# Kernel optimization log

Hardware: AMD Instinct MI355X
Metric: run time of the kernel (lower is better)

Reference implementation:

```python
import jax, jax.numpy as jnp
import numpy as np

N_NODES = 100000
N_EDGES = 1600000
EMB = 64       # embedding_dim
HID = 128      # hidden_channels
N_GRAPHS = 512
N_TASKS = 128
ATOM_VOCAB = 119
BOND_VOCAB = 16


def setup_inputs() -> dict:
    key = jax.random.key(0)
    ks = jax.random.split(key, 24)
    s = 0.02
    inp = {
        'x_idx': jax.random.randint(ks[0], (N_NODES,), 0, ATOM_VOCAB),
        'edge_index': jax.random.randint(ks[1], (2, N_EDGES), 0, N_NODES),
        'edge_attr_idx': jax.random.randint(ks[2], (N_EDGES,), 0, BOND_VOCAB),
        'batch': jnp.sort(jax.random.randint(ks[3], (N_NODES,), 0, N_GRAPHS)),
        'atom_emb': jax.random.normal(ks[4], (ATOM_VOCAB, EMB), jnp.float32) * s,
        'bond_emb': jax.random.normal(ks[5], (BOND_VOCAB, EMB), jnp.float32) * s,
        'w_edge0': jax.random.normal(ks[6], (EMB, EMB), jnp.float32) * s,
        'b_edge0': jnp.zeros((EMB,), jnp.float32),
        'w1_0': jax.random.normal(ks[7], (EMB, HID), jnp.float32) * s,
        'b1_0': jnp.zeros((HID,), jnp.float32),
        'w2_0': jax.random.normal(ks[8], (HID, HID), jnp.float32) * s,
        'b2_0': jnp.zeros((HID,), jnp.float32),
        'w_edge1': jax.random.normal(ks[9], (EMB, HID), jnp.float32) * s,
        'b_edge1': jnp.zeros((HID,), jnp.float32),
        'w1_1': jax.random.normal(ks[10], (HID, HID), jnp.float32) * s,
        'b1_1': jnp.zeros((HID,), jnp.float32),
        'w2_1': jax.random.normal(ks[11], (HID, HID), jnp.float32) * s,
        'b2_1': jnp.zeros((HID,), jnp.float32),
        'lin1_w': jax.random.normal(ks[12], (HID, HID), jnp.float32) * s,
        'lin1_b': jnp.zeros((HID,), jnp.float32),
        'lin2_w': jax.random.normal(ks[13], (HID, N_TASKS), jnp.float32) * s,
        'lin2_b': jnp.zeros((N_TASKS,), jnp.float32),
    }
    return inp


def _gine_conv(x, e, src, dst, we, be, w1, b1, w2, b2):
    # message: relu(x_j + Linear(edge_attr)); aggregate: scatter-add at dst
    msg = jax.nn.relu(x[src] + e @ we + be)            # [E, in_dim]
    agg = jax.ops.segment_sum(msg, dst, num_segments=N_NODES)
    h = x + agg                                        # (1+eps)*x with eps=0
    h = jax.nn.elu(h @ w1 + b1) @ w2 + b2              # GINE nn MLP
    return jax.nn.elu(h)                               # outer F.elu


def reference(x_idx, edge_index, edge_attr_idx, batch,
              atom_emb, bond_emb,
              w_edge0, b_edge0, w1_0, b1_0, w2_0, b2_0,
              w_edge1, b_edge1, w1_1, b1_1, w2_1, b2_1,
              lin1_w, lin1_b, lin2_w, lin2_b):
    x = atom_emb[x_idx]                                # [N, EMB]
    e = bond_emb[edge_attr_idx]                        # [E, EMB]
    src, dst = edge_index[0], edge_index[1]            # flow: source->target
    x = _gine_conv(x, e, src, dst, w_edge0, b_edge0, w1_0, b1_0, w2_0, b2_0)
    x = _gine_conv(x, e, src, dst, w_edge1, b_edge1, w1_1, b1_1, w2_1, b2_1)
    hg = jax.ops.segment_sum(x, batch, num_segments=N_GRAPHS)  # global_add_pool
    hg = jax.nn.relu(hg @ lin1_w + lin1_b)
    return hg @ lin2_w + lin2_b                        # [G, num_tasks]
```

## Files before the change

kernel.cpp:

```cpp
#include <hip/hip_runtime.h>
#include <hip/hip_bf16.h>

static const int NN = 100000;
static const int NE = 1600000;
static const int NG = 512;
static const int NB = 391;
static const int NBLK = 98;

typedef __attribute__((ext_vector_type(8))) short shortx8;
typedef __attribute__((ext_vector_type(4))) float floatx4;

__device__ __forceinline__ float bf2f(unsigned short u) {
  union { unsigned int i; float f; } v; v.i = ((unsigned int)u) << 16; return v.f;
}
__device__ __forceinline__ unsigned short f2bf(float f) {
  union { float f; unsigned int i; } v; v.f = f;
  return (unsigned short)((v.i + 0x7FFFu + ((v.i >> 16) & 1u)) >> 16);
}

__global__ void k_bhist(const int* __restrict__ dst, int* __restrict__ part) {
  __shared__ int cnt[NB];
  for (int i = threadIdx.x; i < NB; i += 256) cnt[i] = 0;
  __syncthreads();
  int base = blockIdx.x * 16384;
  for (int k = 0; k < 64; ++k) {
    int e = base + k * 256 + threadIdx.x;
    if (e < NE) atomicAdd(&cnt[dst[e] >> 8], 1);
  }
  __syncthreads();
  for (int i = threadIdx.x; i < NB; i += 256) part[i * NBLK + blockIdx.x] = cnt[i];
}

__global__ void k_bscan(const int* __restrict__ part, int* __restrict__ bo,
                        int* __restrict__ bcursor, int* __restrict__ offs,
                        unsigned int* __restrict__ csr0, unsigned int* __restrict__ csr1) {
  __shared__ int sh[512];
  int t = threadIdx.x;
  int c0 = 0, c1 = 0;
  if (t < NB) { const int* p = part + t * NBLK; for (int k = 0; k < NBLK; ++k) c0 += p[k]; }
  int u = t + 256;
  if (u < NB) { const int* p = part + u * NBLK; for (int k = 0; k < NBLK; ++k) c1 += p[k]; }
  sh[t] = c0; sh[t + 256] = c1;
  __syncthreads();
  for (int d = 1; d < 512; d <<= 1) {
    int v0 = (t >= d) ? sh[t - d] : 0;
    int v1 = (t + 256 >= d) ? sh[t + 256 - d] : 0;
    __syncthreads();
    sh[t] += v0; sh[t + 256] += v1;
    __syncthreads();
  }
  if (t < NB) { int e0 = sh[t] - c0; bo[t] = e0; bcursor[t] = e0; }
  if (u < NB) { int e0 = sh[u] - c1; bo[u] = e0; bcursor[u] = e0; }
  if (t == 0) offs[NN] = NE;
  if (t < 8) { csr0[NE + t] = 0u; csr1[NE + t] = 0u; }
}

__global__ void k_bin(const int* __restrict__ src, const int* __restrict__ dstp,
                      const int* __restrict__ ea, const int* __restrict__ x_idx,
                      int* __restrict__ bcursor, uint2* __restrict__ pairs) {
  __shared__ int cnt[512];
  __shared__ int incl[512];
  __shared__ int cur[NB];
  __shared__ int rbase[NB];
  __shared__ uint2 stage[4096];
  int t = threadIdx.x;
  int e0 = blockIdx.x * 4096;
  int ecnt = NE - e0; if (ecnt > 4096) ecnt = 4096;
  cnt[t] = 0; cnt[t + 256] = 0;
  __syncthreads();
  for (int k = 0; k < 16; ++k) {
    int i = k * 256 + t;
    if (i < ecnt) atomicAdd(&cnt[dstp[e0 + i] >> 8], 1);
  }
  __syncthreads();
  incl[t] = cnt[t]; incl[t + 256] = cnt[t + 256];
  __syncthreads();
  for (int d = 1; d < 512; d <<= 1) {
    int v0 = (t >= d) ? incl[t - d] : 0;
    int v1 = (t + 256 >= d) ? incl[t + 256 - d] : 0;
    __syncthreads();
    incl[t] += v0; incl[t + 256] += v1;
    __syncthreads();
  }
  if (t < NB) { cur[t] = incl[t] - cnt[t]; if (cnt[t]) rbase[t] = atomicAdd(&bcursor[t], cnt[t]); }
  int u = t + 256;
  if (u < NB) { cur[u] = incl[u] - cnt[u]; if (cnt[u]) rbase[u] = atomicAdd(&bcursor[u], cnt[u]); }
  __syncthreads();
  for (int k = 0; k < 16; ++k) {
    int i = k * 256 + t;
    if (i < ecnt) {
      int e = e0 + i;
      int d = dstp[e];
      int s = src[e];
      unsigned int pk = (unsigned int)s | ((unsigned int)(x_idx[s] * 16 + ea[e]) << 17);
      int p = atomicAdd(&cur[d >> 8], 1);
      stage[p] = make_uint2((unsigned int)d, pk);
    }
  }
  __syncthreads();
  for (int j = t; j < ecnt; j += 256) {
    int lo = 0, hi = NB - 1;
    while (lo < hi) { int mid = (lo + hi) >> 1; if (incl[mid] > j) hi = mid; else lo = mid + 1; }
    int excl = incl[lo] - cnt[lo];
    pairs[rbase[lo] + (j - excl)] = stage[j];
  }
}

__global__ void k_fine(const uint2* __restrict__ pairs, const int* __restrict__ bo,
                       int* __restrict__ offs,
                       unsigned int* __restrict__ csr0, unsigned int* __restrict__ csr1) {
  __shared__ int cnt[256];
  __shared__ int incl[256];
  __shared__ int cur[256];
  int b = blockIdx.x;
  int t = threadIdx.x;
  int start = bo[b];
  int end = (b == NB - 1) ? NE : bo[b + 1];
  int base_n = b << 8;
  cnt[t] = 0;
  __syncthreads();
  for (int j = start + t; j < end; j += 256)
    atomicAdd(&cnt[(int)pairs[j].x - base_n], 1);
  __syncthreads();
  incl[t] = cnt[t];
  __syncthreads();
  for (int d = 1; d < 256; d <<= 1) {
    int v = (t >= d) ? incl[t - d] : 0;
    __syncthreads();
    incl[t] += v;
    __syncthreads();
  }
  int excl = incl[t] - cnt[t];
  cur[t] = excl;
  int node = base_n + t;
  if (node < NN) offs[node] = start + excl;
  __syncthreads();
  for (int j = start + t; j < end; j += 256) {
    uint2 p = pairs[j];
    int pos = start + atomicAdd(&cur[(int)p.x - base_n], 1);
    unsigned int pk = p.y;
    unsigned int idx17 = pk >> 17;
    csr0[pos] = idx17 << 8;
    csr1[pos] = ((pk & 0x1FFFFu) << 8) | (idx17 & 15u);
  }
}

__global__ void k_prep(const float* __restrict__ bond,
                       const float* __restrict__ we0, const float* __restrict__ be0,
                       const float* __restrict__ we1, const float* __restrict__ be1,
                       const float* __restrict__ atom,
                       float* __restrict__ et1, float* __restrict__ M0,
                       const float* __restrict__ s0, const float* __restrict__ s1,
                       const float* __restrict__ s2, const float* __restrict__ s3,
                       const float* __restrict__ s4, const float* __restrict__ s5,
                       unsigned short* __restrict__ d0, unsigned short* __restrict__ d1,
                       unsigned short* __restrict__ d2, unsigned short* __restrict__ d3,
                       unsigned short* __restrict__ d4, unsigned short* __restrict__ d5) {
  int blk = blockIdx.x, t = threadIdx.x;
  if (blk < 8) {
    int i = blk * 256 + t;
    int b = i >> 7, c = i & 127;
    float acc = be1[c];
    for (int k = 0; k < 64; ++k) acc += bond[b * 64 + k] * we1[k * 128 + c];
    et1[i] = acc;
  } else if (blk < 484) {
    int i = (blk - 8) * 256 + t;
    int c = i & 63, b = (i >> 6) & 15, a = i >> 10;
    float acc = be0[c];
    for (int k = 0; k < 64; ++k) acc += bond[b * 64 + k] * we0[k * 64 + c];
    acc += atom[a * 64 + c];
    M0[i] = acc > 0.f ? acc : 0.f;
  } else {
    int task = (blk - 484) >> 6;
    int i = ((blk - 484) & 63) * 256 + t;
    const float* w; unsigned short* wz; int K;
    switch (task) {
      case 0: w = s0; wz = d0; K = 64; break;
      case 1: w = s1; wz = d1; K = 128; break;
      case 2: w = s2; wz = d2; K = 128; break;
      case 3: w = s3; wz = d3; K = 128; break;
      case 4: w = s4; wz = d4; K = 128; break;
      default: w = s5; wz = d5; K = 128; break;
    }
    if (i >= K * 128) return;
    int j = i & 7, lane = (i >> 3) & 63, ct = (i >> 9) & 7, s = i >> 12;
    int k = s * 32 + (lane >> 4) * 8 + j;
    int m = ct * 16 + (lane & 15);
    wz[i] = f2bf(w[k * 128 + m]);
  }
}

__global__ __launch_bounds__(256) void k_agg0(
    const int* __restrict__ x_idx, const float* __restrict__ atom,
    const float* __restrict__ M0, const int* __restrict__ offs,
    const unsigned int* __restrict__ csr0, unsigned short* __restrict__ h0) {
  int t = threadIdx.x, lane = t & 63;
  int n = __builtin_amdgcn_readfirstlane(blockIdx.x * 4 + (t >> 6));
  if (n >= NN) return;
  int s = offs[n], e = offs[n + 1];
  const char* Mb = (const char*)M0;
  unsigned int voff = (unsigned int)lane * 4u;
  float acc = *(const float*)((const char*)atom + ((size_t)(unsigned)x_idx[n] << 8) + voff);
  for (int i = s; i < e; i += 8) {
    unsigned int q0 = csr0[i + 0], q1 = csr0[i + 1], q2 = csr0[i + 2], q3 = csr0[i + 3];
    unsigned int q4 = csr0[i + 4], q5 = csr0[i + 5], q6 = csr0[i + 6], q7 = csr0[i + 7];
    float m1 = (i + 1 < e) ? 1.f : 0.f, m2 = (i + 2 < e) ? 1.f : 0.f;
    float m3 = (i + 3 < e) ? 1.f : 0.f, m4 = (i + 4 < e) ? 1.f : 0.f;
    float m5 = (i + 5 < e) ? 1.f : 0.f, m6 = (i + 6 < e) ? 1.f : 0.f;
    float m7 = (i + 7 < e) ? 1.f : 0.f;
    float v0 = *(const float*)(Mb + q0 + voff);
    float v1 = *(const float*)(Mb + q1 + voff);
    float v2 = *(const float*)(Mb + q2 + voff);
    float v3 = *(const float*)(Mb + q3 + voff);
    float v4 = *(const float*)(Mb + q4 + voff);
    float v5 = *(const float*)(Mb + q5 + voff);
    float v6 = *(const float*)(Mb + q6 + voff);
    float v7 = *(const float*)(Mb + q7 + voff);
    acc += v0;
    acc = fmaf(m1, v1, acc); acc = fmaf(m2, v2, acc);
    acc = fmaf(m3, v3, acc); acc = fmaf(m4, v4, acc);
    acc = fmaf(m5, v5, acc); acc = fmaf(m6, v6, acc);
    acc = fmaf(m7, v7, acc);
  }
  h0[(size_t)n * 64 + lane] = f2bf(acc);
}

__global__ __launch_bounds__(256) void k_agg1(
    const unsigned short* __restrict__ x1, const float* __restrict__ et1,
    const int* __restrict__ offs, const unsigned int* __restrict__ csr1,
    unsigned short* __restrict__ h1) {
  __shared__ float etl[2048];
  int t = threadIdx.x;
#pragma unroll
  for (int k = 0; k < 8; ++k) etl[k * 256 + t] = et1[k * 256 + t];
  __syncthreads();
  int lane = t & 63;
  int n = __builtin_amdgcn_readfirstlane(blockIdx.x * 4 + (t >> 6));
  if (n >= NN) return;
  int s = offs[n], e = offs[n + 1];
  const char* xb = (const char*)x1;
  unsigned int voff = (unsigned int)lane * 4u;
  const char* etb = (const char*)etl + (size_t)lane * 8u;
  unsigned int xv = *(const unsigned int*)(xb + ((size_t)(unsigned)n << 8) + voff);
  float ax = bf2f((unsigned short)(xv & 0xFFFF));
  float ay = bf2f((unsigned short)(xv >> 16));
  for (int i = s; i < e; i += 8) {
    unsigned int q0 = csr1[i + 0], q1 = csr1[i + 1], q2 = csr1[i + 2], q3 = csr1[i + 3];
    unsigned int q4 = csr1[i + 4], q5 = csr1[i + 5], q6 = csr1[i + 6], q7 = csr1[i + 7];
    float m1 = (i + 1 < e) ? 1.f : 0.f, m2 = (i + 2 < e) ? 1.f : 0.f;
    float m3 = (i + 3 < e) ? 1.f : 0.f, m4 = (i + 4 < e) ? 1.f : 0.f;
    float m5 = (i + 5 < e) ? 1.f : 0.f, m6 = (i + 6 < e) ? 1.f : 0.f;
    float m7 = (i + 7 < e) ? 1.f : 0.f;
    unsigned int v0 = *(const unsigned int*)(xb + (q0 & 0xFFFFFF00u) + voff);
    unsigned int v1 = *(const unsigned int*)(xb + (q1 & 0xFFFFFF00u) + voff);
    unsigned int v2 = *(const unsigned int*)(xb + (q2 & 0xFFFFFF00u) + voff);
    unsigned int v3 = *(const unsigned int*)(xb + (q3 & 0xFFFFFF00u) + voff);
    unsigned int v4 = *(const unsigned int*)(xb + (q4 & 0xFFFFFF00u) + voff);
    unsigned int v5 = *(const unsigned int*)(xb + (q5 & 0xFFFFFF00u) + voff);
    unsigned int v6 = *(const unsigned int*)(xb + (q6 & 0xFFFFFF00u) + voff);
    unsigned int v7 = *(const unsigned int*)(xb + (q7 & 0xFFFFFF00u) + voff);
    float2 e0 = *(const float2*)(etb + ((q0 & 15u) << 9));
    float2 e1 = *(const float2*)(etb + ((q1 & 15u) << 9));
    float2 e2 = *(const float2*)(etb + ((q2 & 15u) << 9));
    float2 e3 = *(const float2*)(etb + ((q3 & 15u) << 9));
    float2 e4 = *(const float2*)(etb + ((q4 & 15u) << 9));
    float2 e5 = *(const float2*)(etb + ((q5 & 15u) << 9));
    float2 e6 = *(const float2*)(etb + ((q6 & 15u) << 9));
    float2 e7 = *(const float2*)(etb + ((q7 & 15u) << 9));
    float mx, my;
    mx = bf2f((unsigned short)(v0 & 0xFFFF)) + e0.x; my = bf2f((unsigned short)(v0 >> 16)) + e0.y;
    ax += fmaxf(mx, 0.f); ay += fmaxf(my, 0.f);
    mx = bf2f((unsigned short)(v1 & 0xFFFF)) + e1.x; my = bf2f((unsigned short)(v1 >> 16)) + e1.y;
    ax = fmaf(m1, fmaxf(mx, 0.f), ax); ay = fmaf(m1, fmaxf(my, 0.f), ay);
    mx = bf2f((unsigned short)(v2 & 0xFFFF)) + e2.x; my = bf2f((unsigned short)(v2 >> 16)) + e2.y;
    ax = fmaf(m2, fmaxf(mx, 0.f), ax); ay = fmaf(m2, fmaxf(my, 0.f), ay);
    mx = bf2f((unsigned short)(v3 & 0xFFFF)) + e3.x; my = bf2f((unsigned short)(v3 >> 16)) + e3.y;
    ax = fmaf(m3, fmaxf(mx, 0.f), ax); ay = fmaf(m3, fmaxf(my, 0.f), ay);
    mx = bf2f((unsigned short)(v4 & 0xFFFF)) + e4.x; my = bf2f((unsigned short)(v4 >> 16)) + e4.y;
    ax = fmaf(m4, fmaxf(mx, 0.f), ax); ay = fmaf(m4, fmaxf(my, 0.f), ay);
    mx = bf2f((unsigned short)(v5 & 0xFFFF)) + e5.x; my = bf2f((unsigned short)(v5 >> 16)) + e5.y;
    ax = fmaf(m5, fmaxf(mx, 0.f), ax); ay = fmaf(m5, fmaxf(my, 0.f), ay);
    mx = bf2f((unsigned short)(v6 & 0xFFFF)) + e6.x; my = bf2f((unsigned short)(v6 >> 16)) + e6.y;
    ax = fmaf(m6, fmaxf(mx, 0.f), ax); ay = fmaf(m6, fmaxf(my, 0.f), ay);
    mx = bf2f((unsigned short)(v7 & 0xFFFF)) + e7.x; my = bf2f((unsigned short)(v7 >> 16)) + e7.y;
    ax = fmaf(m7, fmaxf(mx, 0.f), ax); ay = fmaf(m7, fmaxf(my, 0.f), ay);
  }
  unsigned int o = (unsigned int)f2bf(ax) | ((unsigned int)f2bf(ay) << 16);
  *(unsigned int*)(h1 + (size_t)n * 128 + lane * 2) = o;
}

__global__ void k_mlp(const unsigned short* __restrict__ in, int K1,
                      const unsigned short* __restrict__ w1z, const float* __restrict__ b1,
                      const unsigned short* __restrict__ w2z, const float* __restrict__ b2,
                      unsigned short* __restrict__ outb, float* __restrict__ outf,
                      int N, int act1, int act2) {
  __shared__ unsigned short tls[4][16][136];
  int lane = threadIdx.x & 63;
  int wave = threadIdx.x >> 6;
  int row0 = blockIdx.x * 64 + wave * 16;
  int rlo = lane & 15, quad = lane >> 4;
  int arow = row0 + rlo;

  floatx4 acc[8];
#pragma unroll
  for (int ct = 0; ct < 8; ++ct) { acc[ct][0]=0.f; acc[ct][1]=0.f; acc[ct][2]=0.f; acc[ct][3]=0.f; }
  int NS = K1 >> 5;
  for (int s = 0; s < NS; ++s) {
    shortx8 a = {0,0,0,0,0,0,0,0};
    if (arow < N) a = *(const shortx8*)(in + (size_t)arow * K1 + s * 32 + quad * 8);
    const unsigned short* wp = w1z + ((size_t)(s * 8) * 64 + lane) * 8;
#pragma unroll
    for (int ct = 0; ct < 8; ++ct) {
      shortx8 b = *(const shortx8*)(wp + ct * 512);
      acc[ct] = __builtin_amdgcn_mfma_f32_16x16x32_bf16(a, b, acc[ct], 0, 0, 0);
    }
  }
#pragma unroll
  for (int ct = 0; ct < 8; ++ct) {
    float bm = b1[ct * 16 + rlo];
#pragma unroll
    for (int r = 0; r < 4; ++r) {
      float v = acc[ct][r] + bm;
      if (act1 == 1) v = v > 0.f ? v : (__expf(v) - 1.f);
      else if (act1 == 2) v = v > 0.f ? v : 0.f;
      tls[wave][quad * 4 + r][ct * 16 + rlo] = f2bf(v);
    }
  }
  __syncthreads();

  floatx4 acc2[8];
#pragma unroll
  for (int ct = 0; ct < 8; ++ct) { acc2[ct][0]=0.f; acc2[ct][1]=0.f; acc2[ct][2]=0.f; acc2[ct][3]=0.f; }
#pragma unroll
  for (int s = 0; s < 4; ++s) {
    shortx8 a = *(const shortx8*)&tls[wave][rlo][s * 32 + quad * 8];
    const unsigned short* wp = w2z + ((size_t)(s * 8) * 64 + lane) * 8;
#pragma unroll
    for (int ct = 0; ct < 8; ++ct) {
      shortx8 b = *(const shortx8*)(wp + ct * 512);
      acc2[ct] = __builtin_amdgcn_mfma_f32_16x16x32_bf16(a, b, acc2[ct], 0, 0, 0);
    }
  }
#pragma unroll
  for (int ct = 0; ct < 8; ++ct) {
    float bm = b2[ct * 16 + rlo];
#pragma unroll
    for (int r = 0; r < 4; ++r) {
      int rr = row0 + quad * 4 + r;
      if (rr < N) {
        float v = acc2[ct][r] + bm;
        if (act2 == 1) v = v > 0.f ? v : (__expf(v) - 1.f);
        else if (act2 == 2) v = v > 0.f ? v : 0.f;
        if (outb) outb[(size_t)rr * 128 + ct * 16 + rlo] = f2bf(v);
        else outf[(size_t)rr * 128 + ct * 16 + rlo] = v;
      }
    }
  }
}

__global__ __launch_bounds__(256) void k_pool(
    const unsigned short* __restrict__ x2, const int* __restrict__ batch,
    float* __restrict__ hgf) {
  int gt = blockIdx.x * 256 + threadIdx.x;
  int chunk = gt >> 6, lane = gt & 63;
  int n0 = chunk * 32;
  if (n0 >= NN) return;
  int nend = n0 + 32; if (nend > NN) nend = NN;
  float ax = 0.f, ay = 0.f;
  const unsigned short* xp = x2 + lane * 2;
  int gcur = batch[n0];
  for (int n = n0; n < nend; ++n) {
    int g = batch[n];
    if (g != gcur) {
      atomicAdd(&hgf[gcur * 128 + lane * 2], ax);
      atomicAdd(&hgf[gcur * 128 + lane * 2 + 1], ay);
      ax = 0.f; ay = 0.f; gcur = g;
    }
    unsigned int v = *(const unsigned int*)(xp + (size_t)n * 128);
    ax += bf2f((unsigned short)(v & 0xFFFF));
    ay += bf2f((unsigned short)(v >> 16));
  }
  atomicAdd(&hgf[gcur * 128 + lane * 2], ax);
  atomicAdd(&hgf[gcur * 128 + lane * 2 + 1], ay);
}

__global__ void k_head(const float* __restrict__ in,
                       const unsigned short* __restrict__ w1z, const float* __restrict__ b1,
                       const unsigned short* __restrict__ w2z, const float* __restrict__ b2,
                       float* __restrict__ outf, int N) {
  __shared__ unsigned short tls[4][16][136];
  int lane = threadIdx.x & 63;
  int wave = threadIdx.x >> 6;
  int row0 = blockIdx.x * 64 + wave * 16;
  int rlo = lane & 15, quad = lane >> 4;
  int arow = row0 + rlo;
  floatx4 acc[8];
#pragma unroll
  for (int ct = 0; ct < 8; ++ct) { acc[ct][0]=0.f; acc[ct][1]=0.f; acc[ct][2]=0.f; acc[ct][3]=0.f; }
#pragma unroll
  for (int s = 0; s < 4; ++s) {
    shortx8 a = {0,0,0,0,0,0,0,0};
    if (arow < N) {
      const float* rp = in + (size_t)arow * 128 + s * 32 + quad * 8;
      float4 f0 = *(const float4*)rp;
      float4 f1 = *(const float4*)(rp + 4);
      a[0] = (short)f2bf(f0.x); a[1] = (short)f2bf(f0.y);
      a[2] = (short)f2bf(f0.z); a[3] = (short)f2bf(f0.w);
      a[4] = (short)f2bf(f1.x); a[5] = (short)f2bf(f1.y);
      a[6] = (short)f2bf(f1.z); a[7] = (short)f2bf(f1.w);
    }
    const unsigned short* wp = w1z + ((size_t)(s * 8) * 64 + lane) * 8;
#pragma unroll
    for (int ct = 0; ct < 8; ++ct) {
      shortx8 b = *(const shortx8*)(wp + ct * 512);
      acc[ct] = __builtin_amdgcn_mfma_f32_16x16x32_bf16(a, b, acc[ct], 0, 0, 0);
    }
  }
#pragma unroll
  for (int ct = 0; ct < 8; ++ct) {
    float bm = b1[ct * 16 + rlo];
#pragma unroll
    for (int r = 0; r < 4; ++r) {
      float v = acc[ct][r] + bm;
      v = v > 0.f ? v : 0.f;
      tls[wave][quad * 4 + r][ct * 16 + rlo] = f2bf(v);
    }
  }
  __syncthreads();
  floatx4 acc2[8];
#pragma unroll
  for (int ct = 0; ct < 8; ++ct) { acc2[ct][0]=0.f; acc2[ct][1]=0.f; acc2[ct][2]=0.f; acc2[ct][3]=0.f; }
#pragma unroll
  for (int s = 0; s < 4; ++s) {
    shortx8 a = *(const shortx8*)&tls[wave][rlo][s * 32 + quad * 8];
    const unsigned short* wp = w2z + ((size_t)(s * 8) * 64 + lane) * 8;
#pragma unroll
    for (int ct = 0; ct < 8; ++ct) {
      shortx8 b = *(const shortx8*)(wp + ct * 512);
      acc2[ct] = __builtin_amdgcn_mfma_f32_16x16x32_bf16(a, b, acc2[ct], 0, 0, 0);
    }
  }
#pragma unroll
  for (int ct = 0; ct < 8; ++ct) {
    float bm = b2[ct * 16 + rlo];
#pragma unroll
    for (int r = 0; r < 4; ++r) {
      int rr = row0 + quad * 4 + r;
      if (rr < N) outf[(size_t)rr * 128 + ct * 16 + rlo] = acc2[ct][r] + bm;
    }
  }
}

extern "C" void kernel_launch(void* const* d_in, const int* in_sizes, int n_in,
                              void* d_out, int out_size, void* d_ws, size_t ws_size,
                              hipStream_t stream) {
  const int* x_idx  = (const int*)d_in[0];
  const int* e_src  = (const int*)d_in[1];
  const int* e_dst  = e_src + NE;
  const int* e_attr = (const int*)d_in[2];
  const int* batch  = (const int*)d_in[3];
  const float* atom = (const float*)d_in[4];
  const float* bond = (const float*)d_in[5];
  const float* we0  = (const float*)d_in[6];
  const float* be0  = (const float*)d_in[7];
  const float* w1_0 = (const float*)d_in[8];
  const float* b1_0 = (const float*)d_in[9];
  const float* w2_0 = (const float*)d_in[10];
  const float* b2_0 = (const float*)d_in[11];
  const float* we1  = (const float*)d_in[12];
  const float* be1  = (const float*)d_in[13];
  const float* w1_1 = (const float*)d_in[14];
  const float* b1_1 = (const float*)d_in[15];
  const float* w2_1 = (const float*)d_in[16];
  const float* b2_1 = (const float*)d_in[17];
  const float* l1w  = (const float*)d_in[18];
  const float* l1b  = (const float*)d_in[19];
  const float* l2w  = (const float*)d_in[20];
  const float* l2b  = (const float*)d_in[21];

  char* ws = (char*)d_ws;
  size_t off = 0;
  auto alloc = [&](size_t bytes) -> void* {
    void* p = ws + off;
    off = (off + bytes + 255) & ~(size_t)255;
    return p;
  };
  int* part    = (int*)alloc((size_t)NB * NBLK * 4);
  int* bo      = (int*)alloc((size_t)NB * 4);
  int* bcursor = (int*)alloc((size_t)NB * 4);
  int* offs    = (int*)alloc((size_t)(NN + 1) * 4);
  float* et1   = (float*)alloc(16 * 128 * 4);
  float* M0    = (float*)alloc((size_t)119 * 16 * 64 * 4);
  unsigned short* w1_0z = (unsigned short*)alloc(64 * 128 * 2);
  unsigned short* w2_0z = (unsigned short*)alloc(128 * 128 * 2);
  unsigned short* w1_1z = (unsigned short*)alloc(128 * 128 * 2);
  unsigned short* w2_1z = (unsigned short*)alloc(128 * 128 * 2);
  unsigned short* l1z   = (unsigned short*)alloc(128 * 128 * 2);
  unsigned short* l2z   = (unsigned short*)alloc(128 * 128 * 2);
  uint2* pairs = (uint2*)alloc((size_t)NE * 8);
  unsigned int* csr0 = (unsigned int*)alloc(((size_t)NE + 8) * 4);
  unsigned int* csr1 = (unsigned int*)alloc(((size_t)NE + 8) * 4);
  unsigned short* x1 = (unsigned short*)alloc((size_t)NN * 128 * 2);
  unsigned short* h1 = (unsigned short*)alloc((size_t)NN * 128 * 2);
  float* hgf = (float*)alloc((size_t)NG * 128 * 4);
  unsigned short* h0 = (unsigned short*)pairs;
  unsigned short* x2 = x1;

  hipMemsetAsync(hgf, 0, (size_t)NG * 128 * 4, stream);

  k_bhist<<<NBLK, 256, 0, stream>>>(e_dst, part);
  k_bscan<<<1, 256, 0, stream>>>(part, bo, bcursor, offs, csr0, csr1);
  k_bin<<<(NE + 4095) / 4096, 256, 0, stream>>>(e_src, e_dst, e_attr, x_idx, bcursor, pairs);
  k_fine<<<NB, 256, 0, stream>>>(pairs, bo, offs, csr0, csr1);
  k_prep<<<868, 256, 0, stream>>>(bond, we0, be0, we1, be1, atom, et1, M0,
                                  w1_0, w2_0, w1_1, w2_1, l1w, l2w,
                                  w1_0z, w2_0z, w1_1z, w2_1z, l1z, l2z);
  k_agg0<<<NN / 4, 256, 0, stream>>>(x_idx, atom, M0, offs, csr0, h0);
  k_mlp<<<(NN + 63) / 64, 256, 0, stream>>>(h0, 64, w1_0z, b1_0, w2_0z, b2_0,
                                            x1, nullptr, NN, 1, 1);
  k_agg1<<<NN / 4, 256, 0, stream>>>(x1, et1, offs, csr1, h1);
  k_mlp<<<(NN + 63) / 64, 256, 0, stream>>>(h1, 128, w1_1z, b1_1, w2_1z, b2_1,
                                            x2, nullptr, NN, 1, 1);
  k_pool<<<(((NN + 31) / 32) * 64 + 255) / 256, 256, 0, stream>>>(x2, batch, hgf);
  k_head<<<(NG + 63) / 64, 256, 0, stream>>>(hgf, l1z, l1b, l2z, l2b, (float*)d_out, NG);
}
```

Measured before the change: 372.0 us.

## Pad CSR segments to multiples of eight with sentinel edges, fuse histogram into prep

Each node's CSR segment is padded up to a multiple of 8 entries. The padding slots point to sentinel rows: a zero row in M0, and a -1e30 row in the edge table so relu gives zero. This removes the per-edge mask multiplies in both aggregation kernels, and a global atomic cursor assigns the padded segment bases. The dst histogram is merged into the prep kernel to save a launch, and the bin scatter now takes the bucket from the key instead of a binary search. The MLP also stages its input tile in shared memory. The cost is up to 7 extra gathers per node and a larger CSR footprint.

```diff
diff --git a/kernel.cpp b/kernel.cpp
--- a/kernel.cpp
+++ b/kernel.cpp
@@ -6,6 +6,7 @@
 static const int NG = 512;
 static const int NB = 391;
 static const int NBLK = 98;
+static const int CSRM = 2400000;
 
 typedef __attribute__((ext_vector_type(8))) short shortx8;
 typedef __attribute__((ext_vector_type(4))) float floatx4;
@@ -18,22 +19,66 @@
   return (unsigned short)((v.i + 0x7FFFu + ((v.i >> 16) & 1u)) >> 16);
 }
 
-__global__ void k_bhist(const int* __restrict__ dst, int* __restrict__ part) {
+__global__ void k_prep(const int* __restrict__ dst, int* __restrict__ part,
+                       const float* __restrict__ bond,
+                       const float* __restrict__ we0, const float* __restrict__ be0,
+                       const float* __restrict__ we1, const float* __restrict__ be1,
+                       const float* __restrict__ atom,
+                       float* __restrict__ et1, float* __restrict__ M0,
+                       const float* __restrict__ s0, const float* __restrict__ s1,
+                       const float* __restrict__ s2, const float* __restrict__ s3,
+                       const float* __restrict__ s4, const float* __restrict__ s5,
+                       unsigned short* __restrict__ d0, unsigned short* __restrict__ d1,
+                       unsigned short* __restrict__ d2, unsigned short* __restrict__ d3,
+                       unsigned short* __restrict__ d4, unsigned short* __restrict__ d5) {
   __shared__ int cnt[NB];
-  for (int i = threadIdx.x; i < NB; i += 256) cnt[i] = 0;
-  __syncthreads();
-  int base = blockIdx.x * 16384;
-  for (int k = 0; k < 64; ++k) {
-    int e = base + k * 256 + threadIdx.x;
-    if (e < NE) atomicAdd(&cnt[dst[e] >> 8], 1);
-  }
-  __syncthreads();
-  for (int i = threadIdx.x; i < NB; i += 256) part[i * NBLK + blockIdx.x] = cnt[i];
+  int blk = blockIdx.x, t = threadIdx.x;
+  if (blk < NBLK) {
+    for (int i = t; i < NB; i += 256) cnt[i] = 0;
+    __syncthreads();
+    int base = blk * 16384;
+    for (int k = 0; k < 64; ++k) {
+      int e = base + k * 256 + t;
+      if (e < NE) atomicAdd(&cnt[dst[e] >> 8], 1);
+    }
+    __syncthreads();
+    for (int i = t; i < NB; i += 256) part[i * NBLK + blk] = cnt[i];
+  } else if (blk < 106) {
+    int i = (blk - 98) * 256 + t;
+    int b = i >> 7, c = i & 127;
+    float acc = be1[c];
+    for (int k = 0; k < 64; ++k) acc += bond[b * 64 + k] * we1[k * 128 + c];
+    et1[i] = acc;
+  } else if (blk < 582) {
+    int i = (blk - 106) * 256 + t;
+    int c = i & 63, b = (i >> 6) & 15, a = i >> 10;
+    float acc = be0[c];
+    for (int k = 0; k < 64; ++k) acc += bond[b * 64 + k] * we0[k * 64 + c];
+    acc += atom[a * 64 + c];
+    M0[i] = acc > 0.f ? acc : 0.f;
+  } else {
+    int task = (blk - 582) >> 6;
+    int i = ((blk - 582) & 63) * 256 + t;
+    const float* w; unsigned short* wz; int K;
+    switch (task) {
+      case 0: w = s0; wz = d0; K = 64; break;
+      case 1: w = s1; wz = d1; K = 128; break;
+      case 2: w = s2; wz = d2; K = 128; break;
+      case 3: w = s3; wz = d3; K = 128; break;
+      case 4: w = s4; wz = d4; K = 128; break;
+      default: w = s5; wz = d5; K = 128; break;
+    }
+    if (i >= K * 128) return;
+    int j = i & 7, lane = (i >> 3) & 63, ct = (i >> 9) & 7, s = i >> 12;
+    int k = s * 32 + (lane >> 4) * 8 + j;
+    int m = ct * 16 + (lane & 15);
+    wz[i] = f2bf(w[k * 128 + m]);
+  }
 }
 
 __global__ void k_bscan(const int* __restrict__ part, int* __restrict__ bo,
-                        int* __restrict__ bcursor, int* __restrict__ offs,
-                        unsigned int* __restrict__ csr0, unsigned int* __restrict__ csr1) {
+                        int* __restrict__ bcursor, int* __restrict__ gcursor,
+                        float* __restrict__ M0) {
   __shared__ int sh[512];
   int t = threadIdx.x;
   int c0 = 0, c1 = 0;
@@ -51,8 +96,8 @@
   }
   if (t < NB) { int e0 = sh[t] - c0; bo[t] = e0; bcursor[t] = e0; }
   if (u < NB) { int e0 = sh[u] - c1; bo[u] = e0; bcursor[u] = e0; }
-  if (t == 0) offs[NN] = NE;
-  if (t < 8) { csr0[NE + t] = 0u; csr1[NE + t] = 0u; }
+  if (t == 0) *gcursor = 0;
+  if (t < 64) M0[1904 * 64 + t] = 0.f;
 }
 
 __global__ void k_bin(const int* __restrict__ src, const int* __restrict__ dstp,
@@ -99,19 +144,21 @@
   }
   __syncthreads();
   for (int j = t; j < ecnt; j += 256) {
-    int lo = 0, hi = NB - 1;
-    while (lo < hi) { int mid = (lo + hi) >> 1; if (incl[mid] > j) hi = mid; else lo = mid + 1; }
-    int excl = incl[lo] - cnt[lo];
-    pairs[rbase[lo] + (j - excl)] = stage[j];
+    uint2 p = stage[j];
+    int b = (int)(p.x >> 8);
+    int excl = incl[b] - cnt[b];
+    pairs[rbase[b] + (j - excl)] = p;
   }
 }
 
 __global__ void k_fine(const uint2* __restrict__ pairs, const int* __restrict__ bo,
-                       int* __restrict__ offs,
+                       int* __restrict__ gcursor, int* __restrict__ offs,
+                       int* __restrict__ cnts,
                        unsigned int* __restrict__ csr0, unsigned int* __restrict__ csr1) {
   __shared__ int cnt[256];
   __shared__ int incl[256];
   __shared__ int cur[256];
+  __shared__ int sbase;
   int b = blockIdx.x;
   int t = threadIdx.x;
   int start = bo[b];
@@ -122,7 +169,8 @@
   for (int j = start + t; j < end; j += 256)
     atomicAdd(&cnt[(int)pairs[j].x - base_n], 1);
   __syncthreads();
-  incl[t] = cnt[t];
+  int pc = (cnt[t] + 7) & ~7;
+  incl[t] = pc;
   __syncthreads();
   for (int d = 1; d < 256; d <<= 1) {
     int v = (t >= d) ? incl[t - d] : 0;
@@ -130,84 +178,44 @@
     incl[t] += v;
     __syncthreads();
   }
-  int excl = incl[t] - cnt[t];
-  cur[t] = excl;
+  if (t == 255) sbase = atomicAdd(gcursor, incl[255]);
+  __syncthreads();
+  int base = sbase;
+  int pexcl = incl[t] - pc;
+  cur[t] = pexcl;
   int node = base_n + t;
-  if (node < NN) offs[node] = start + excl;
+  if (node < NN) { offs[node] = base + pexcl; cnts[node] = pc; }
   __syncthreads();
   for (int j = start + t; j < end; j += 256) {
     uint2 p = pairs[j];
-    int pos = start + atomicAdd(&cur[(int)p.x - base_n], 1);
+    int pos = base + atomicAdd(&cur[(int)p.x - base_n], 1);
     unsigned int pk = p.y;
     unsigned int idx17 = pk >> 17;
     csr0[pos] = idx17 << 8;
     csr1[pos] = ((pk & 0x1FFFFu) << 8) | (idx17 & 15u);
   }
-}
-
-__global__ void k_prep(const float* __restrict__ bond,
-                       const float* __restrict__ we0, const float* __restrict__ be0,
-                       const float* __restrict__ we1, const float* __restrict__ be1,
-                       const float* __restrict__ atom,
-                       float* __restrict__ et1, float* __restrict__ M0,
-                       const float* __restrict__ s0, const float* __restrict__ s1,
-                       const float* __restrict__ s2, const float* __restrict__ s3,
-                       const float* __restrict__ s4, const float* __restrict__ s5,
-                       unsigned short* __restrict__ d0, unsigned short* __restrict__ d1,
-                       unsigned short* __restrict__ d2, unsigned short* __restrict__ d3,
-                       unsigned short* __restrict__ d4, unsigned short* __restrict__ d5) {
-  int blk = blockIdx.x, t = threadIdx.x;
-  if (blk < 8) {
-    int i = blk * 256 + t;
-    int b = i >> 7, c = i & 127;
-    float acc = be1[c];
-    for (int k = 0; k < 64; ++k) acc += bond[b * 64 + k] * we1[k * 128 + c];
-    et1[i] = acc;
-  } else if (blk < 484) {
-    int i = (blk - 8) * 256 + t;
-    int c = i & 63, b = (i >> 6) & 15, a = i >> 10;
-    float acc = be0[c];
-    for (int k = 0; k < 64; ++k) acc += bond[b * 64 + k] * we0[k * 64 + c];
-    acc += atom[a * 64 + c];
-    M0[i] = acc > 0.f ? acc : 0.f;
-  } else {
-    int task = (blk - 484) >> 6;
-    int i = ((blk - 484) & 63) * 256 + t;
-    const float* w; unsigned short* wz; int K;
-    switch (task) {
-      case 0: w = s0; wz = d0; K = 64; break;
-      case 1: w = s1; wz = d1; K = 128; break;
-      case 2: w = s2; wz = d2; K = 128; break;
-      case 3: w = s3; wz = d3; K = 128; break;
-      case 4: w = s4; wz = d4; K = 128; break;
-      default: w = s5; wz = d5; K = 128; break;
-    }
-    if (i >= K * 128) return;
-    int j = i & 7, lane = (i >> 3) & 63, ct = (i >> 9) & 7, s = i >> 12;
-    int k = s * 32 + (lane >> 4) * 8 + j;
-    int m = ct * 16 + (lane & 15);
-    wz[i] = f2bf(w[k * 128 + m]);
+  __syncthreads();
+  for (int k = cur[t]; k < incl[t]; ++k) {
+    csr0[base + k] = 1904u << 8;
+    csr1[base + k] = 16u;
   }
 }
 
 __global__ __launch_bounds__(256) void k_agg0(
     const int* __restrict__ x_idx, const float* __restrict__ atom,
     const float* __restrict__ M0, const int* __restrict__ offs,
+    const int* __restrict__ cnts,
     const unsigned int* __restrict__ csr0, unsigned short* __restrict__ h0) {
   int t = threadIdx.x, lane = t & 63;
   int n = __builtin_amdgcn_readfirstlane(blockIdx.x * 4 + (t >> 6));
   if (n >= NN) return;
-  int s = offs[n], e = offs[n + 1];
+  int s = offs[n], e = s + cnts[n];
   const char* Mb = (const char*)M0;
   unsigned int voff = (unsigned int)lane * 4u;
   float acc = *(const float*)((const char*)atom + ((size_t)(unsigned)x_idx[n] << 8) + voff);
   for (int i = s; i < e; i += 8) {
     unsigned int q0 = csr0[i + 0], q1 = csr0[i + 1], q2 = csr0[i + 2], q3 = csr0[i + 3];
     unsigned int q4 = csr0[i + 4], q5 = csr0[i + 5], q6 = csr0[i + 6], q7 = csr0[i + 7];
-    float m1 = (i + 1 < e) ? 1.f : 0.f, m2 = (i + 2 < e) ? 1.f : 0.f;
-    float m3 = (i + 3 < e) ? 1.f : 0.f, m4 = (i + 4 < e) ? 1.f : 0.f;
-    float m5 = (i + 5 < e) ? 1.f : 0.f, m6 = (i + 6 < e) ? 1.f : 0.f;
-    float m7 = (i + 7 < e) ? 1.f : 0.f;
     float v0 = *(const float*)(Mb + q0 + voff);
     float v1 = *(const float*)(Mb + q1 + voff);
     float v2 = *(const float*)(Mb + q2 + voff);
@@ -216,28 +224,28 @@
     float v5 = *(const float*)(Mb + q5 + voff);
     float v6 = *(const float*)(Mb + q6 + voff);
     float v7 = *(const float*)(Mb + q7 + voff);
-    acc += v0;
-    acc = fmaf(m1, v1, acc); acc = fmaf(m2, v2, acc);
-    acc = fmaf(m3, v3, acc); acc = fmaf(m4, v4, acc);
-    acc = fmaf(m5, v5, acc); acc = fmaf(m6, v6, acc);
-    acc = fmaf(m7, v7, acc);
+    acc += ((v0 + v1) + (v2 + v3)) + ((v4 + v5) + (v6 + v7));
   }
   h0[(size_t)n * 64 + lane] = f2bf(acc);
 }
 
 __global__ __launch_bounds__(256) void k_agg1(
     const unsigned short* __restrict__ x1, const float* __restrict__ et1,
-    const int* __restrict__ offs, const unsigned int* __restrict__ csr1,
-    unsigned short* __restrict__ h1) {
-  __shared__ float etl[2048];
+    const int* __restrict__ offs, const int* __restrict__ cnts,
+    const unsigned int* __restrict__ csr1, unsigned short* __restrict__ h1) {
+  __shared__ float etl[17 * 128];
   int t = threadIdx.x;
 #pragma unroll
-  for (int k = 0; k < 8; ++k) etl[k * 256 + t] = et1[k * 256 + t];
+  for (int k = 0; k < 9; ++k) {
+    int idx = k * 256 + t;
+    if (idx < 2048) etl[idx] = et1[idx];
+    else if (idx < 2176) etl[idx] = -1e30f;
+  }
   __syncthreads();
   int lane = t & 63;
   int n = __builtin_amdgcn_readfirstlane(blockIdx.x * 4 + (t >> 6));
   if (n >= NN) return;
-  int s = offs[n], e = offs[n + 1];
+  int s = offs[n], e = s + cnts[n];
   const char* xb = (const char*)x1;
   unsigned int voff = (unsigned int)lane * 4u;
   const char* etb = (const char*)etl + (size_t)lane * 8u;
@@ -247,10 +255,6 @@
   for (int i = s; i < e; i += 8) {
     unsigned int q0 = csr1[i + 0], q1 = csr1[i + 1], q2 = csr1[i + 2], q3 = csr1[i + 3];
     unsigned int q4 = csr1[i + 4], q5 = csr1[i + 5], q6 = csr1[i + 6], q7 = csr1[i + 7];
-    float m1 = (i + 1 < e) ? 1.f : 0.f, m2 = (i + 2 < e) ? 1.f : 0.f;
-    float m3 = (i + 3 < e) ? 1.f : 0.f, m4 = (i + 4 < e) ? 1.f : 0.f;
-    float m5 = (i + 5 < e) ? 1.f : 0.f, m6 = (i + 6 < e) ? 1.f : 0.f;
-    float m7 = (i + 7 < e) ? 1.f : 0.f;
     unsigned int v0 = *(const unsigned int*)(xb + (q0 & 0xFFFFFF00u) + voff);
     unsigned int v1 = *(const unsigned int*)(xb + (q1 & 0xFFFFFF00u) + voff);
     unsigned int v2 = *(const unsigned int*)(xb + (q2 & 0xFFFFFF00u) + voff);
@@ -259,31 +263,31 @@
     unsigned int v5 = *(const unsigned int*)(xb + (q5 & 0xFFFFFF00u) + voff);
     unsigned int v6 = *(const unsigned int*)(xb + (q6 & 0xFFFFFF00u) + voff);
     unsigned int v7 = *(const unsigned int*)(xb + (q7 & 0xFFFFFF00u) + voff);
-    float2 e0 = *(const float2*)(etb + ((q0 & 15u) << 9));
-    float2 e1 = *(const float2*)(etb + ((q1 & 15u) << 9));
-    float2 e2 = *(const float2*)(etb + ((q2 & 15u) << 9));
-    float2 e3 = *(const float2*)(etb + ((q3 & 15u) << 9));
-    float2 e4 = *(const float2*)(etb + ((q4 & 15u) << 9));
-    float2 e5 = *(const float2*)(etb + ((q5 & 15u) << 9));
-    float2 e6 = *(const float2*)(etb + ((q6 & 15u) << 9));
-    float2 e7 = *(const float2*)(etb + ((q7 & 15u) << 9));
+    float2 e0 = *(const float2*)(etb + ((q0 & 31u) << 9));
+    float2 e1 = *(const float2*)(etb + ((q1 & 31u) << 9));
+    float2 e2 = *(const float2*)(etb + ((q2 & 31u) << 9));
+    float2 e3 = *(const float2*)(etb + ((q3 & 31u) << 9));
+    float2 e4 = *(const float2*)(etb + ((q4 & 31u) << 9));
+    float2 e5 = *(const float2*)(etb + ((q5 & 31u) << 9));
+    float2 e6 = *(const float2*)(etb + ((q6 & 31u) << 9));
+    float2 e7 = *(const float2*)(etb + ((q7 & 31u) << 9));
     float mx, my;
     mx = bf2f((unsigned short)(v0 & 0xFFFF)) + e0.x; my = bf2f((unsigned short)(v0 >> 16)) + e0.y;
     ax += fmaxf(mx, 0.f); ay += fmaxf(my, 0.f);
     mx = bf2f((unsigned short)(v1 & 0xFFFF)) + e1.x; my = bf2f((unsigned short)(v1 >> 16)) + e1.y;
-    ax = fmaf(m1, fmaxf(mx, 0.f), ax); ay = fmaf(m1, fmaxf(my, 0.f), ay);
+    ax += fmaxf(mx, 0.f); ay += fmaxf(my, 0.f);
     mx = bf2f((unsigned short)(v2 & 0xFFFF)) + e2.x; my = bf2f((unsigned short)(v2 >> 16)) + e2.y;
-    ax = fmaf(m2, fmaxf(mx, 0.f), ax); ay = fmaf(m2, fmaxf(my, 0.f), ay);
+    ax += fmaxf(mx, 0.f); ay += fmaxf(my, 0.f);
     mx = bf2f((unsigned short)(v3 & 0xFFFF)) + e3.x; my = bf2f((unsigned short)(v3 >> 16)) + e3.y;
-    ax = fmaf(m3, fmaxf(mx, 0.f), ax); ay = fmaf(m3, fmaxf(my, 0.f), ay);
+    ax += fmaxf(mx, 0.f); ay += fmaxf(my, 0.f);
     mx = bf2f((unsigned short)(v4 & 0xFFFF)) + e4.x; my = bf2f((unsigned short)(v4 >> 16)) + e4.y;
-    ax = fmaf(m4, fmaxf(mx, 0.f), ax); ay = fmaf(m4, fmaxf(my, 0.f), ay);
+    ax += fmaxf(mx, 0.f); ay += fmaxf(my, 0.f);
     mx = bf2f((unsigned short)(v5 & 0xFFFF)) + e5.x; my = bf2f((unsigned short)(v5 >> 16)) + e5.y;
-    ax = fmaf(m5, fmaxf(mx, 0.f), ax); ay = fmaf(m5, fmaxf(my, 0.f), ay);
+    ax += fmaxf(mx, 0.f); ay += fmaxf(my, 0.f);
     mx = bf2f((unsigned short)(v6 & 0xFFFF)) + e6.x; my = bf2f((unsigned short)(v6 >> 16)) + e6.y;
-    ax = fmaf(m6, fmaxf(mx, 0.f), ax); ay = fmaf(m6, fmaxf(my, 0.f), ay);
+    ax += fmaxf(mx, 0.f); ay += fmaxf(my, 0.f);
     mx = bf2f((unsigned short)(v7 & 0xFFFF)) + e7.x; my = bf2f((unsigned short)(v7 >> 16)) + e7.y;
-    ax = fmaf(m7, fmaxf(mx, 0.f), ax); ay = fmaf(m7, fmaxf(my, 0.f), ay);
+    ax += fmaxf(mx, 0.f); ay += fmaxf(my, 0.f);
   }
   unsigned int o = (unsigned int)f2bf(ax) | ((unsigned int)f2bf(ay) << 16);
   *(unsigned int*)(h1 + (size_t)n * 128 + lane * 2) = o;
@@ -294,20 +298,30 @@
                       const unsigned short* __restrict__ w2z, const float* __restrict__ b2,
                       unsigned short* __restrict__ outb, float* __restrict__ outf,
                       int N, int act1, int act2) {
+  __shared__ unsigned short tileA[64][136];
   __shared__ unsigned short tls[4][16][136];
-  int lane = threadIdx.x & 63;
-  int wave = threadIdx.x >> 6;
-  int row0 = blockIdx.x * 64 + wave * 16;
+  int t = threadIdx.x;
+  int lane = t & 63, wave = t >> 6;
+  int row0b = blockIdx.x * 64;
+  int lg = (K1 == 64) ? 3 : 4;
+  int cpr = 1 << lg;
+  int nch = 64 << lg;
+  shortx8 zero = {0, 0, 0, 0, 0, 0, 0, 0};
+  for (int c = t; c < nch; c += 256) {
+    int r = c >> lg, col = c & (cpr - 1);
+    shortx8 v = zero;
+    if (row0b + r < N) v = *(const shortx8*)(in + (size_t)(row0b + r) * K1 + col * 8);
+    *(shortx8*)&tileA[r][col * 8] = v;
+  }
+  __syncthreads();
+  int row0 = row0b + wave * 16;
   int rlo = lane & 15, quad = lane >> 4;
-  int arow = row0 + rlo;
-
   floatx4 acc[8];
 #pragma unroll
   for (int ct = 0; ct < 8; ++ct) { acc[ct][0]=0.f; acc[ct][1]=0.f; acc[ct][2]=0.f; acc[ct][3]=0.f; }
   int NS = K1 >> 5;
   for (int s = 0; s < NS; ++s) {
-    shortx8 a = {0,0,0,0,0,0,0,0};
-    if (arow < N) a = *(const shortx8*)(in + (size_t)arow * K1 + s * 32 + quad * 8);
+    shortx8 a = *(const shortx8*)&tileA[wave * 16 + rlo][s * 32 + quad * 8];
     const unsigned short* wp = w1z + ((size_t)(s * 8) * 64 + lane) * 8;
 #pragma unroll
     for (int ct = 0; ct < 8; ++ct) {
@@ -327,7 +341,6 @@
     }
   }
   __syncthreads();
-
   floatx4 acc2[8];
 #pragma unroll
   for (int ct = 0; ct < 8; ++ct) { acc2[ct][0]=0.f; acc2[ct][1]=0.f; acc2[ct][2]=0.f; acc2[ct][3]=0.f; }
@@ -488,9 +501,11 @@
   int* part    = (int*)alloc((size_t)NB * NBLK * 4);
   int* bo      = (int*)alloc((size_t)NB * 4);
   int* bcursor = (int*)alloc((size_t)NB * 4);
-  int* offs    = (int*)alloc((size_t)(NN + 1) * 4);
+  int* gcursor = (int*)alloc(256);
+  int* offs    = (int*)alloc((size_t)NN * 4);
+  int* cnts    = (int*)alloc((size_t)NN * 4);
   float* et1   = (float*)alloc(16 * 128 * 4);
-  float* M0    = (float*)alloc((size_t)119 * 16 * 64 * 4);
+  float* M0    = (float*)alloc((size_t)1905 * 64 * 4);
   unsigned short* w1_0z = (unsigned short*)alloc(64 * 128 * 2);
   unsigned short* w2_0z = (unsigned short*)alloc(128 * 128 * 2);
   unsigned short* w1_1z = (unsigned short*)alloc(128 * 128 * 2);
@@ -498,8 +513,8 @@
   unsigned short* l1z   = (unsigned short*)alloc(128 * 128 * 2);
   unsigned short* l2z   = (unsigned short*)alloc(128 * 128 * 2);
   uint2* pairs = (uint2*)alloc((size_t)NE * 8);
-  unsigned int* csr0 = (unsigned int*)alloc(((size_t)NE + 8) * 4);
-  unsigned int* csr1 = (unsigned int*)alloc(((size_t)NE + 8) * 4);
+  unsigned int* csr0 = (unsigned int*)alloc((size_t)CSRM * 4);
+  unsigned int* csr1 = (unsigned int*)alloc((size_t)CSRM * 4);
   unsigned short* x1 = (unsigned short*)alloc((size_t)NN * 128 * 2);
   unsigned short* h1 = (unsigned short*)alloc((size_t)NN * 128 * 2);
   float* hgf = (float*)alloc((size_t)NG * 128 * 4);
@@ -508,17 +523,16 @@
 
   hipMemsetAsync(hgf, 0, (size_t)NG * 128 * 4, stream);
 
-  k_bhist<<<NBLK, 256, 0, stream>>>(e_dst, part);
-  k_bscan<<<1, 256, 0, stream>>>(part, bo, bcursor, offs, csr0, csr1);
-  k_bin<<<(NE + 4095) / 4096, 256, 0, stream>>>(e_src, e_dst, e_attr, x_idx, bcursor, pairs);
-  k_fine<<<NB, 256, 0, stream>>>(pairs, bo, offs, csr0, csr1);
-  k_prep<<<868, 256, 0, stream>>>(bond, we0, be0, we1, be1, atom, et1, M0,
+  k_prep<<<966, 256, 0, stream>>>(e_dst, part, bond, we0, be0, we1, be1, atom, et1, M0,
                                   w1_0, w2_0, w1_1, w2_1, l1w, l2w,
                                   w1_0z, w2_0z, w1_1z, w2_1z, l1z, l2z);
-  k_agg0<<<NN / 4, 256, 0, stream>>>(x_idx, atom, M0, offs, csr0, h0);
+  k_bscan<<<1, 256, 0, stream>>>(part, bo, bcursor, gcursor, M0);
+  k_bin<<<(NE + 4095) / 4096, 256, 0, stream>>>(e_src, e_dst, e_attr, x_idx, bcursor, pairs);
+  k_fine<<<NB, 256, 0, stream>>>(pairs, bo, gcursor, offs, cnts, csr0, csr1);
+  k_agg0<<<NN / 4, 256, 0, stream>>>(x_idx, atom, M0, offs, cnts, csr0, h0);
   k_mlp<<<(NN + 63) / 64, 256, 0, stream>>>(h0, 64, w1_0z, b1_0, w2_0z, b2_0,
                                             x1, nullptr, NN, 1, 1);
-  k_agg1<<<NN / 4, 256, 0, stream>>>(x1, et1, offs, csr1, h1);
+  k_agg1<<<NN / 4, 256, 0, stream>>>(x1, et1, offs, cnts, csr1, h1);
   k_mlp<<<(NN + 63) / 64, 256, 0, stream>>>(h1, 128, w1_1z, b1_1, w2_1z, b2_1,
                                             x2, nullptr, NN, 1, 1);
   k_pool<<<(((NN + 31) / 32) * 64 + 255) / 256, 256, 0, stream>>>(x2, batch, hgf);
```

Measured after the change: 404.1 us. 1.09x slower.
